# Performance work log

Measured on AMD Instinct MI355X. Metric: run time of the kernel, lower is better.

## Reference

```python
import jax, jax.numpy as jnp
import numpy as np


def setup_inputs() -> dict:
    key = jax.random.key(0)
    k1, k2, k3 = jax.random.split(key, 3)
    B, S, DB, DW, W = 64, 512, 768, 100, 512
    bert_x = jax.random.normal(k1, (B, S, DB), dtype=jnp.float32)
    w2v_input = jax.random.normal(k2, (B, W, DW), dtype=jnp.float32)
    mappings = jax.random.randint(k3, (B, S - 1), 0, W, dtype=jnp.int32)
    return {"bert_x": bert_x, "w2v_input": w2v_input, "mappings": mappings}


def reference(bert_x, w2v_input, mappings):
    # bert_x: [B, S, DB] (frozen SciBERT last_hidden_state)
    # w2v_input: [B, W, DW] (FastText word vectors)
    # mappings: [B, S-1] int; loop breaks at first -1, writes row i+1
    B, S, DB = bert_x.shape
    DW = w2v_input.shape[2]
    dt = bert_x.dtype
    # loop-break semantics: valid only while all previous mappings != -1
    valid = jnp.cumprod((mappings != -1).astype(jnp.int32), axis=1).astype(dt)  # [B, S-1]
    safe = jnp.clip(mappings, 0)
    w2v_g = jnp.take_along_axis(w2v_input, safe[..., None], axis=1)  # [B, S-1, DW]
    body = jnp.concatenate(
        [bert_x[:, 1:, :] * valid[..., None], w2v_g * valid[..., None]], axis=-1
    )  # [B, S-1, DB+DW]
    zero_row = jnp.zeros((B, 1, DB + DW), dtype=dt)  # CLS row stays zero
    return jnp.concatenate([zero_row, body], axis=1)  # [B, S, DB+DW]
```

## Files before the change

kernel.cpp:

```cpp
#include <hip/hip_runtime.h>
#include <hip/hip_bf16.h>


#define B_   64
#define S_   512
#define SM1_ 511
#define DB_  768
#define DW_  100
#define DOUT_ 868
#define DOUT4_ 217
#define DB4_  192
#define W_   512

__global__ void first_invalid_kernel(const int* __restrict__ mappings,
                                     int* __restrict__ firstinv) {
    const int b = blockIdx.x;
    __shared__ int s_min;
    if (threadIdx.x == 0) s_min = SM1_;
    __syncthreads();
    for (int i = threadIdx.x; i < SM1_; i += blockDim.x) {
        if (mappings[b * SM1_ + i] == -1) atomicMin(&s_min, i);
    }
    __syncthreads();
    if (threadIdx.x == 0) firstinv[b] = s_min;
}

__global__ void fuse_rows_kernel(const float* __restrict__ bert_x,
                                 const float* __restrict__ w2v,
                                 const int* __restrict__ mappings,
                                 const int* __restrict__ firstinv,
                                 float* __restrict__ out) {
    const int row = blockIdx.x;
    const int b = row >> 9;
    const int r = row & (S_ - 1);
    const int tid = threadIdx.x;
    float4* orow = reinterpret_cast<float4*>(out + (size_t)row * DOUT_);

    bool valid = false;
    if (r != 0) {
        valid = (r - 1) < firstinv[b];
    }
    if (!valid) {
        if (tid < DOUT4_) orow[tid] = make_float4(0.f, 0.f, 0.f, 0.f);
        return;
    }

    if (tid < DB4_) {
        const float4* brow = reinterpret_cast<const float4*>(
            bert_x + ((size_t)b * S_ + r) * DB_);
        orow[tid] = brow[tid];
    } else if (tid < DOUT4_) {
        int w = mappings[b * SM1_ + (r - 1)];
        if (w < 0) w = 0;
        const float4* wrow = reinterpret_cast<const float4*>(
            w2v + ((size_t)b * W_ + w) * DW_);
        orow[tid] = wrow[tid - DB4_];
    }
}

extern "C" void kernel_launch(void* const* d_in, const int* in_sizes, int n_in,
                              void* d_out, int out_size, void* d_ws, size_t ws_size,
                              hipStream_t stream) {
    const float* bert_x = (const float*)d_in[0];
    const float* w2v    = (const float*)d_in[1];
    const int* mappings = (const int*)d_in[2];
    float* out = (float*)d_out;
    int* firstinv = (int*)d_ws;

    first_invalid_kernel<<<B_, 512, 0, stream>>>(mappings, firstinv);
    fuse_rows_kernel<<<B_ * S_, 256, 0, stream>>>(bert_x, w2v, mappings, firstinv, out);
}
```

Baseline: 43.29 us.

## Fuse first-invalid scan into row-copy kernel and process eight rows per block

Removes the separate first-invalid kernel launch. Each block now recomputes the per-batch first -1 index from the mappings row in shared memory, then copies eight output rows instead of one. This saves a launch and the dependency between the two kernels and cuts the block count eightfold, at the cost of every block redundantly scanning 511 mapping entries and a barrier before any copy starts.

After: 40.39 us. 6.7% less time.

```diff
diff --git a/kernel.cpp b/kernel.cpp
--- a/kernel.cpp
+++ b/kernel.cpp
@@ -2,59 +2,60 @@
 #include <hip/hip_bf16.h>
 
 
-#define B_   64
-#define S_   512
-#define SM1_ 511
-#define DB_  768
-#define DW_  100
+#define B_    64
+#define S_    512
+#define SM1_  511
+#define DB_   768
+#define DW_   100
 #define DOUT_ 868
 #define DOUT4_ 217
 #define DB4_  192
-#define W_   512
+#define W_    512
+#define ROWS_PER_BLK_ 8
 
-__global__ void first_invalid_kernel(const int* __restrict__ mappings,
-                                     int* __restrict__ firstinv) {
-    const int b = blockIdx.x;
+__global__ __launch_bounds__(256) void fused_fuse_rows_kernel(
+        const float* __restrict__ bert_x,
+        const float* __restrict__ w2v,
+        const int* __restrict__ mappings,
+        float* __restrict__ out) {
+    const int blk   = blockIdx.x;
+    const int b     = blk >> 6;
+    const int chunk = blk & 63;
+    const int r0    = chunk * ROWS_PER_BLK_;
+    const int tid   = threadIdx.x;
+
     __shared__ int s_min;
-    if (threadIdx.x == 0) s_min = SM1_;
+    if (tid == 0) s_min = SM1_;
     __syncthreads();
-    for (int i = threadIdx.x; i < SM1_; i += blockDim.x) {
-        if (mappings[b * SM1_ + i] == -1) atomicMin(&s_min, i);
+    const int* __restrict__ mrow = mappings + b * SM1_;
+    #pragma unroll
+    for (int i = tid; i < SM1_; i += 256) {
+        if (mrow[i] == -1) atomicMin(&s_min, i);
     }
     __syncthreads();
-    if (threadIdx.x == 0) firstinv[b] = s_min;
-}
+    const int fi = s_min;
 
-__global__ void fuse_rows_kernel(const float* __restrict__ bert_x,
-                                 const float* __restrict__ w2v,
-                                 const int* __restrict__ mappings,
-                                 const int* __restrict__ firstinv,
-                                 float* __restrict__ out) {
-    const int row = blockIdx.x;
-    const int b = row >> 9;
-    const int r = row & (S_ - 1);
-    const int tid = threadIdx.x;
-    float4* orow = reinterpret_cast<float4*>(out + (size_t)row * DOUT_);
+    const float4* __restrict__ bbase = reinterpret_cast<const float4*>(
+        bert_x + (size_t)b * S_ * DB_);
+    const float4* __restrict__ wbase = reinterpret_cast<const float4*>(
+        w2v + (size_t)b * W_ * DW_);
+    float4* __restrict__ obase = reinterpret_cast<float4*>(
+        out + (size_t)b * S_ * DOUT_);
 
-    bool valid = false;
-    if (r != 0) {
-        valid = (r - 1) < firstinv[b];
-    }
-    if (!valid) {
-        if (tid < DOUT4_) orow[tid] = make_float4(0.f, 0.f, 0.f, 0.f);
-        return;
-    }
-
-    if (tid < DB4_) {
-        const float4* brow = reinterpret_cast<const float4*>(
-            bert_x + ((size_t)b * S_ + r) * DB_);
-        orow[tid] = brow[tid];
-    } else if (tid < DOUT4_) {
-        int w = mappings[b * SM1_ + (r - 1)];
-        if (w < 0) w = 0;
-        const float4* wrow = reinterpret_cast<const float4*>(
-            w2v + ((size_t)b * W_ + w) * DW_);
-        orow[tid] = wrow[tid - DB4_];
+    #pragma unroll
+    for (int rr = 0; rr < ROWS_PER_BLK_; ++rr) {
+        const int r = r0 + rr;
+        float4* orow = obase + (size_t)r * DOUT4_;
+        const bool valid = (r != 0) && ((r - 1) < fi);
+        if (!valid) {
+            if (tid < DOUT4_) orow[tid] = make_float4(0.f, 0.f, 0.f, 0.f);
+        } else if (tid < DB4_) {
+            orow[tid] = bbase[(size_t)r * DB4_ + tid];
+        } else if (tid < DOUT4_) {
+            int w = mrow[r - 1];
+            if (w < 0) w = 0;
+            orow[tid] = wbase[(size_t)w * (DW_ / 4) + (tid - DB4_)];
+        }
     }
 }
 
@@ -65,8 +66,7 @@
     const float* w2v    = (const float*)d_in[1];
     const int* mappings = (const int*)d_in[2];
     float* out = (float*)d_out;
-    int* firstinv = (int*)d_ws;
 
-    first_invalid_kernel<<<B_, 512, 0, stream>>>(mappings, firstinv);
-    fuse_rows_kernel<<<B_ * S_, 256, 0, stream>>>(bert_x, w2v, mappings, firstinv, out);
+    fused_fuse_rows_kernel<<<B_ * (S_ / ROWS_PER_BLK_), 256, 0, stream>>>(
+        bert_x, w2v, mappings, out);
 }
```
